# Kernel optimization log

Measured on AMD Instinct MI355X. Metric: run time of the kernel, lower is better.

Reference implementation:

```python
import jax, jax.numpy as jnp
import numpy as np


def _bilinear(plane, coords):
    # plane: [B, C, H, W]; coords: [B, N, 2] in [-1, 1]; coords[...,0]->x (W axis), [...,1]->y (H axis)
    # matches F.grid_sample(mode='bilinear', padding_mode='border', align_corners=True)
    B, C, H, W = plane.shape
    x = jnp.clip((coords[..., 0] + 1.0) * 0.5 * (W - 1), 0.0, W - 1)
    y = jnp.clip((coords[..., 1] + 1.0) * 0.5 * (H - 1), 0.0, H - 1)
    x0 = jnp.floor(x)
    y0 = jnp.floor(y)
    x0i = x0.astype(jnp.int32)
    y0i = y0.astype(jnp.int32)
    x1i = jnp.minimum(x0i + 1, W - 1)
    y1i = jnp.minimum(y0i + 1, H - 1)
    wx = (x - x0)[:, :, None]
    wy = (y - y0)[:, :, None]
    pf = plane.reshape(B, C, H * W)

    def g(yi, xi):
        idx = (yi * W + xi)[:, None, :]            # [B,1,N]
        return jnp.take_along_axis(pf, idx, axis=2).transpose(0, 2, 1)  # [B,N,C]

    f00 = g(y0i, x0i)
    f01 = g(y0i, x1i)
    f10 = g(y1i, x0i)
    f11 = g(y1i, x1i)
    return (f00 * (1 - wx) * (1 - wy) + f01 * wx * (1 - wy)
            + f10 * (1 - wx) * wy + f11 * wx * wy)


def _sample(p, c_xz, c_xy, c_yz):
    # project 3D points onto the three canonical planes and sum bilinear features
    return (_bilinear(c_xz, p[..., jnp.array([0, 2])])
            + _bilinear(c_xy, p[..., jnp.array([0, 1])])
            + _bilinear(c_yz, p[..., jnp.array([1, 2])]))


def setup_inputs() -> dict:
    key = jax.random.key(0)
    ks = jax.random.split(key, 10)
    B, N, C, S, H = 8, 4096, 128, 8, 64
    query_pos = jax.random.uniform(ks[0], (B, N, 3), dtype=jnp.float32) * 2.0 - 1.0
    c_xz = jax.random.normal(ks[1], (B, C, H, H), dtype=jnp.float32)
    c_xy = jax.random.normal(ks[2], (B, C, H, H), dtype=jnp.float32)
    c_yz = jax.random.normal(ks[3], (B, C, H, H), dtype=jnp.float32)
    s = C ** -0.5
    Wq = jax.random.normal(ks[4], (C, C), dtype=jnp.float32) * s
    Wk = jax.random.normal(ks[5], (C, C), dtype=jnp.float32) * s
    Wv = jax.random.normal(ks[6], (C, C), dtype=jnp.float32) * s
    Wout = jax.random.normal(ks[7], (C, C), dtype=jnp.float32) * s
    Woff = jax.random.normal(ks[8], (C, 3 * S), dtype=jnp.float32) * s * 0.1  # small offsets
    return dict(query_pos=query_pos, c_xz=c_xz, c_xy=c_xy, c_yz=c_yz,
                Wq=Wq, bq=jnp.zeros((C,), jnp.float32),
                Wk=Wk, bk=jnp.zeros((C,), jnp.float32),
                Wv=Wv, bv=jnp.zeros((C,), jnp.float32),
                Wout=Wout, bout=jnp.zeros((C,), jnp.float32),
                Woff=Woff, boff=jnp.zeros((3 * S,), jnp.float32))


def reference(query_pos, c_xz, c_xy, c_yz, Wq, bq, Wk, bk, Wv, bv,
              Wout, bout, Woff, boff):
    B, N, _ = query_pos.shape
    C = Wq.shape[0]
    S = Woff.shape[1] // 3
    # sample features at query points (bilinear gather from triplanes)
    feature = _sample(query_pos, c_xz, c_xy, c_yz)                     # [B,N,C]
    # learned deformable offsets -> S auxiliary sample points per query
    offset = (feature @ Woff + boff).reshape(B, N, S, 3)
    aux_pts = offset + query_pos[:, :, None, :]                        # [B,N,S,3]
    aux_feat = _sample(aux_pts.reshape(B, N * S, 3),
                       c_xz, c_xy, c_yz).reshape(B, N, S, C)           # [B,N,S,C]
    k = aux_feat @ Wk + bk                                             # [B,N,S,C]
    v = aux_feat @ Wv + bv
    q = feature @ Wq + bq                                              # [B,N,C]
    scale = C ** (-0.5)
    q = q / scale  # faithful to original: q = q / self.scale
    sim = jnp.einsum('bnd,bnjd->bnj', q, k)                            # [B,N,S]
    attn = jax.nn.softmax(sim, axis=-1)
    out = jnp.einsum('bnj,bnjd->bnd', attn, v)                         # [B,N,C]
    out = out @ Wout + bout + feature                                  # residual
    return out
```

## Files before the change

kernel.cpp:

```cpp
#include <hip/hip_runtime.h>
#include <math.h>

#define BB 8
#define NN 4096
#define CC 128
#define SS 8
#define HH 64
#define HW 4096
#define PLANE_B (HW*CC)
#define SQRT_C 11.3137084989847603904f

__global__ __launch_bounds__(128) void transpose_planes(
    const float* __restrict__ pxz, const float* __restrict__ pxy,
    const float* __restrict__ pyz, float* __restrict__ dst) {
  int bid = blockIdx.x;
  int c   = threadIdx.x;
  int hw0 = (bid & 255) * 16;
  int b   = (bid >> 8) & 7;
  int p   = bid >> 11;
  const float* src = (p == 0) ? pxz : (p == 1) ? pxy : pyz;
  const float4* s4 = (const float4*)(src + (size_t)(b * CC + c) * HW + hw0);
  float4 v0 = s4[0], v1 = s4[1], v2 = s4[2], v3 = s4[3];
  float vals[16];
  vals[0]=v0.x; vals[1]=v0.y; vals[2]=v0.z; vals[3]=v0.w;
  vals[4]=v1.x; vals[5]=v1.y; vals[6]=v1.z; vals[7]=v1.w;
  vals[8]=v2.x; vals[9]=v2.y; vals[10]=v2.z; vals[11]=v2.w;
  vals[12]=v3.x; vals[13]=v3.y; vals[14]=v3.z; vals[15]=v3.w;
  float* d = dst + (size_t)(p * BB + b) * PLANE_B + (size_t)hw0 * CC + c;
#pragma unroll
  for (int i = 0; i < 16; ++i) d[i * CC] = vals[i];
}

__device__ __forceinline__ int morton3_3(int cx, int cy, int cz) {
  int m = 0;
#pragma unroll
  for (int k = 0; k < 3; ++k) {
    m |= ((cx >> k) & 1) << (3 * k);
    m |= ((cy >> k) & 1) << (3 * k + 1);
    m |= ((cz >> k) & 1) << (3 * k + 2);
  }
  return m;
}

__global__ __launch_bounds__(1024) void sort_queries(
    const float* __restrict__ qpos, int* __restrict__ sidx) {
  const int b = blockIdx.x;
  const int t = threadIdx.x;
  __shared__ unsigned short scell[NN];
  __shared__ int hist[512];
  __shared__ int tmp[512];
  __shared__ int cur[512];
  if (t < 512) hist[t] = 0;
  __syncthreads();
  for (int i = t; i < NN; i += 1024) {
    const float* qp = qpos + ((size_t)b * NN + i) * 3;
    float x = qp[0], y = qp[1], z = qp[2];
    int cx = min(7, max(0, (int)((x + 1.f) * 4.f)));
    int cy = min(7, max(0, (int)((y + 1.f) * 4.f)));
    int cz = min(7, max(0, (int)((z + 1.f) * 4.f)));
    int cell = morton3_3(cx, cy, cz);
    scell[i] = (unsigned short)cell;
    atomicAdd(&hist[cell], 1);
  }
  __syncthreads();
  if (t < 512) tmp[t] = hist[t];
  __syncthreads();
  for (int off = 1; off < 512; off <<= 1) {
    int v = 0;
    if (t < 512 && t >= off) v = tmp[t - off];
    __syncthreads();
    if (t < 512) tmp[t] += v;
    __syncthreads();
  }
  if (t < 512) cur[t] = tmp[t] - hist[t];
  __syncthreads();
  for (int i = t; i < NN; i += 1024) {
    int cell = scell[i];
    int pos = atomicAdd(&cur[cell], 1);
    sidx[b * NN + pos] = i;
  }
}

__global__ __launch_bounds__(128) void prep_mats(
    const float* __restrict__ Wq, const float* __restrict__ bq,
    const float* __restrict__ Wk,
    const float* __restrict__ Wv, const float* __restrict__ bv,
    const float* __restrict__ Wout, const float* __restrict__ bout,
    const float* __restrict__ Woff,
    float* __restrict__ Mt, float* __restrict__ u,
    float* __restrict__ W2, float* __restrict__ b2,
    float* __restrict__ Wofft) {
  int t = threadIdx.x;
  int blk = blockIdx.x;
  if (blk < 128) {
    __shared__ float lwq[128];
    lwq[t] = Wq[blk * 128 + t];
    __syncthreads();
    float acc = 0.f;
#pragma unroll 8
    for (int d = 0; d < 128; ++d) acc += Wk[t * 128 + d] * lwq[d];
    Mt[blk * 128 + t] = SQRT_C * acc;
  } else if (blk < 256) {
    int c = blk - 128;
    float acc = 0.f;
#pragma unroll 8
    for (int e = 0; e < 128; ++e) acc += Wv[c * 128 + e] * Wout[e * 128 + t];
    W2[c * 128 + t] = acc;
  } else if (blk == 256) {
    float au = 0.f, ab = 0.f;
    for (int d = 0; d < 128; ++d) au += Wk[t * 128 + d] * bq[d];
    u[t] = SQRT_C * au;
    for (int e = 0; e < 128; ++e) ab += bv[e] * Wout[e * 128 + t];
    b2[t] = ab + bout[t];
  } else {
#pragma unroll
    for (int j = 0; j < 24; ++j) Wofft[j * 128 + t] = Woff[t * 24 + j];
  }
}

__device__ __forceinline__ void make_combo(float cx, float cy,
                                           int4* oi, float4* ow) {
  float fx = fminf(fmaxf((cx + 1.f) * 31.5f, 0.f), 63.f);
  float fy = fminf(fmaxf((cy + 1.f) * 31.5f, 0.f), 63.f);
  float x0f = floorf(fx), y0f = floorf(fy);
  int x0 = (int)x0f, y0 = (int)y0f;
  int x1 = min(x0 + 1, 63), y1 = min(y0 + 1, 63);
  float wx = fx - x0f, wy = fy - y0f;
  int r0 = y0 << 15, r1 = y1 << 15;
  int cb0 = x0 << 9, cb1 = x1 << 9;
  *oi = make_int4(r0 + cb0, r0 + cb1, r1 + cb0, r1 + cb1);
  float wxy = wx * wy;
  *ow = make_float4(1.f - wx - wy + wxy, wx - wxy, wy - wxy, wxy);
}

__device__ __forceinline__ float ldf(const char* p, int off) {
  return *(const float*)(p + off);
}

__global__ __launch_bounds__(128, 4) void deform_attn9(
    const float* __restrict__ qpos, const int* __restrict__ sidx,
    const float* __restrict__ pT,
    const float* __restrict__ Mt, const float* __restrict__ u,
    const float* __restrict__ W2, const float* __restrict__ bias2,
    const float* __restrict__ Wofft, const float* __restrict__ boff,
    float* __restrict__ out) {
  const int tid = threadIdx.x;
  const int c = tid;
  const int l = tid & 63;
  const int wv = tid >> 6;
  const int bid = blockIdx.x;
  const int b = bid & 7;
  const int n0 = (bid >> 3) * 8;

  __shared__ int snidx[8];
  __shared__ float spos[24];
  __shared__ int4   sfi[24];
  __shared__ float4 sfw[24];
  __shared__ int4   sci[192];
  __shared__ float4 scw[192];
  __shared__ __align__(16) float sbuf[CC * 8];
  __shared__ float soff[8][24];
  __shared__ float sred[8][2][8];

  if (tid < 8) snidx[tid] = sidx[b * NN + n0 + tid];
  __syncthreads();
  if (tid < 24) {
    int q = tid / 3, comp = tid - q * 3;
    spos[tid] = qpos[((size_t)b * NN + snidx[q]) * 3 + comp];
  }
  __syncthreads();

  const char* pb0 = (const char*)(pT + (size_t)(0 * BB + b) * PLANE_B + c);
  const char* pb1 = (const char*)(pT + (size_t)(1 * BB + b) * PLANE_B + c);
  const char* pb2 = (const char*)(pT + (size_t)(2 * BB + b) * PLANE_B + c);

  if (tid < 24) {
    int p = tid >> 3, q = tid & 7;
    float px = spos[q * 3 + 0], py = spos[q * 3 + 1], pz = spos[q * 3 + 2];
    float cx = (p == 2) ? py : px;
    float cy = (p == 1) ? py : pz;
    make_combo(cx, cy, &sfi[tid], &sfw[tid]);
  }
  __syncthreads();

  float featr[8];
#pragma unroll
  for (int q = 0; q < 8; ++q) {
    float f = 0.f;
#pragma unroll
    for (int p = 0; p < 3; ++p) {
      int4 oi = sfi[p * 8 + q];
      float4 w = sfw[p * 8 + q];
      const char* base = (p == 0) ? pb0 : (p == 1) ? pb1 : pb2;
      f += w.x * ldf(base, oi.x) + w.y * ldf(base, oi.y)
         + w.z * ldf(base, oi.z) + w.w * ldf(base, oi.w);
    }
    featr[q] = f;
    sbuf[c * 8 + q] = f;
  }
  __syncthreads();

  float qk[8];
  {
    float uc = u[c];
#pragma unroll
    for (int q = 0; q < 8; ++q) qk[q] = uc;
#pragma unroll 4
    for (int cp = 0; cp < CC; ++cp) {
      float m = Mt[cp * CC + c];
      float4 f0 = *(const float4*)&sbuf[cp * 8];
      float4 f1 = *(const float4*)&sbuf[cp * 8 + 4];
      qk[0] += m * f0.x; qk[1] += m * f0.y; qk[2] += m * f0.z; qk[3] += m * f0.w;
      qk[4] += m * f1.x; qk[5] += m * f1.y; qk[6] += m * f1.z; qk[7] += m * f1.w;
    }
  }

#pragma unroll
  for (int rep = 0; rep < 2; ++rep) {
    int m = rep * 128 + tid;
    if (m < 192) {
      int q = m / 24;
      int t24 = m - q * 24;
      float acc = boff[t24];
      const float* wrow = Wofft + t24 * 128;
#pragma unroll 4
      for (int cp = 0; cp < CC; ++cp) acc += sbuf[cp * 8 + q] * wrow[cp];
      soff[q][t24] = acc;
    }
  }
  __syncthreads();

#pragma unroll
  for (int rep = 0; rep < 2; ++rep) {
    int m = rep * 128 + tid;
    if (m < 192) {
      int p = m >> 6, q = (m >> 3) & 7, j = m & 7;
      float ox = spos[q * 3 + 0] + soff[q][j * 3 + 0];
      float oy = spos[q * 3 + 1] + soff[q][j * 3 + 1];
      float oz = spos[q * 3 + 2] + soff[q][j * 3 + 2];
      float cx = (p == 2) ? oy : ox;
      float cy = (p == 1) ? oy : oz;
      make_combo(cx, cy, &sci[m], &scw[m]);
    }
  }
  __syncthreads();

  const int lb0 = l & 1, lb1 = (l >> 1) & 1, lb2 = (l >> 2) & 1;
#pragma unroll
  for (int q = 0; q < 8; ++q) {
    float a8[8], part[8];
#pragma unroll
    for (int j = 0; j < 8; ++j) {
      float a = 0.f;
#pragma unroll
      for (int p = 0; p < 3; ++p) {
        int idx = p * 64 + q * 8 + j;
        int4 oi = sci[idx];
        float4 w = scw[idx];
        const char* base = (p == 0) ? pb0 : (p == 1) ? pb1 : pb2;
        a += w.x * ldf(base, oi.x) + w.y * ldf(base, oi.y)
           + w.z * ldf(base, oi.z) + w.w * ldf(base, oi.w);
      }
      a8[j] = a;
      part[j] = a * qk[q];
    }
    float s2[4];
#pragma unroll
    for (int k = 0; k < 4; ++k) {
      float pa = part[2 * k], pb_ = part[2 * k + 1];
      float snd = lb0 ? pa : pb_;
      float kp  = lb0 ? pb_ : pa;
      s2[k] = kp + __shfl_xor(snd, 1);
    }
    float s4[2];
#pragma unroll
    for (int k = 0; k < 2; ++k) {
      float pa = s2[2 * k], pb_ = s2[2 * k + 1];
      float snd = lb1 ? pa : pb_;
      float kp  = lb1 ? pb_ : pa;
      s4[k] = kp + __shfl_xor(snd, 2);
    }
    float s8;
    {
      float snd = lb2 ? s4[0] : s4[1];
      float kp  = lb2 ? s4[1] : s4[0];
      s8 = kp + __shfl_xor(snd, 4);
    }
    s8 += __shfl_xor(s8, 8);
    s8 += __shfl_xor(s8, 16);
    s8 += __shfl_xor(s8, 32);
    if (l < 8) sred[q][wv][l] = s8;
    __syncthreads();
    float sim[8];
#pragma unroll
    for (int j = 0; j < 8; ++j) sim[j] = sred[q][0][j] + sred[q][1][j];
    float mx = fmaxf(fmaxf(fmaxf(sim[0], sim[1]), fmaxf(sim[2], sim[3])),
                     fmaxf(fmaxf(sim[4], sim[5]), fmaxf(sim[6], sim[7])));
    float den = 0.f;
#pragma unroll
    for (int j = 0; j < 8; ++j) { sim[j] = __expf(sim[j] - mx); den += sim[j]; }
    float inv = 1.f / den;
    float w = 0.f;
#pragma unroll
    for (int j = 0; j < 8; ++j) w += sim[j] * a8[j];
    sbuf[c * 8 + q] = w * inv;
  }
  __syncthreads();

  float o[8];
  {
    float bb = bias2[c];
#pragma unroll
    for (int q = 0; q < 8; ++q) o[q] = bb;
#pragma unroll 4
    for (int cp = 0; cp < CC; ++cp) {
      float m = W2[cp * CC + c];
      float4 f0 = *(const float4*)&sbuf[cp * 8];
      float4 f1 = *(const float4*)&sbuf[cp * 8 + 4];
      o[0] += m * f0.x; o[1] += m * f0.y; o[2] += m * f0.z; o[3] += m * f0.w;
      o[4] += m * f1.x; o[5] += m * f1.y; o[6] += m * f1.z; o[7] += m * f1.w;
    }
  }
#pragma unroll
  for (int q = 0; q < 8; ++q) {
    out[((size_t)b * NN + snidx[q]) * CC + c] = o[q] + featr[q];
  }
}

__device__ __forceinline__ float bil(const float* __restrict__ base,
                                     float cx, float cy, int es, int rs) {
  float fx = fminf(fmaxf((cx + 1.f) * 31.5f, 0.f), 63.f);
  float fy = fminf(fmaxf((cy + 1.f) * 31.5f, 0.f), 63.f);
  float x0f = floorf(fx), y0f = floorf(fy);
  int x0 = (int)x0f, y0 = (int)y0f;
  int x1 = min(x0 + 1, 63), y1 = min(y0 + 1, 63);
  float wx = fx - x0f, wy = fy - y0f;
  const float* r0 = base + y0 * rs;
  const float* r1 = base + y1 * rs;
  float f00 = r0[x0 * es], f01 = r0[x1 * es];
  float f10 = r1[x0 * es], f11 = r1[x1 * es];
  float top = f00 + (f01 - f00) * wx;
  float bot = f10 + (f11 - f10) * wx;
  return top + (bot - top) * wy;
}

__global__ __launch_bounds__(128) void deform_attn_fb(
    const float* __restrict__ qpos,
    const float* __restrict__ pxz, const float* __restrict__ pxy,
    const float* __restrict__ pyz,
    const float* __restrict__ Mt, const float* __restrict__ u,
    const float* __restrict__ W2, const float* __restrict__ b2,
    const float* __restrict__ Woff, const float* __restrict__ boff,
    float* __restrict__ out) {
  const int tid = threadIdx.x;
  const int c = tid;
  const int bid = blockIdx.x;
  const int b = bid & 7;
  const int n0 = (bid >> 3) * 8;
  const int es = 1, rs = HH;
  const float* bxz = pxz + (size_t)(b * CC + c) * HW;
  const float* bxy = pxy + (size_t)(b * CC + c) * HW;
  const float* byz = pyz + (size_t)(b * CC + c) * HW;

  __shared__ __align__(16) float sfeat[CC * 8];
  __shared__ __align__(16) float swv[CC * 8];
  __shared__ float spos[24];
  __shared__ float soff[8][24];
  __shared__ float sred[8][2][8];

  if (tid < 24) spos[tid] = qpos[(size_t)(b * NN + n0) * 3 + tid];
  __syncthreads();
#pragma unroll
  for (int q = 0; q < 8; ++q) {
    float px = spos[q*3+0], py = spos[q*3+1], pz = spos[q*3+2];
    sfeat[c*8+q] = bil(bxz,px,pz,es,rs)+bil(bxy,px,py,es,rs)+bil(byz,py,pz,es,rs);
  }
  __syncthreads();
  float qk[8];
  {
    float uc = u[c];
#pragma unroll
    for (int q = 0; q < 8; ++q) qk[q] = uc;
    for (int cp = 0; cp < CC; ++cp) {
      float m = Mt[cp*CC+c];
#pragma unroll
      for (int q = 0; q < 8; ++q) qk[q] += m * sfeat[cp*8+q];
    }
  }
  if (tid < 120) {
    int q = tid/24, j = tid%24;
    float acc = boff[j];
    for (int cp = 0; cp < CC; ++cp) acc += sfeat[cp*8+q]*Woff[cp*24+j];
    soff[q][j] = acc;
  }
  if (tid < 72) {
    int q = 5+tid/24, j = tid%24;
    float acc = boff[j];
    for (int cp = 0; cp < CC; ++cp) acc += sfeat[cp*8+q]*Woff[cp*24+j];
    soff[q][j] = acc;
  }
  __syncthreads();
  const int wvid = tid >> 6;
  for (int q = 0; q < 8; ++q) {
    float px = spos[q*3+0], py = spos[q*3+1], pz = spos[q*3+2];
    float a8[8];
#pragma unroll
    for (int j = 0; j < 8; ++j) {
      float ox = px+soff[q][j*3+0], oy = py+soff[q][j*3+1], oz = pz+soff[q][j*3+2];
      float a = bil(bxz,ox,oz,es,rs)+bil(bxy,ox,oy,es,rs)+bil(byz,oy,oz,es,rs);
      a8[j] = a;
      float p = a * qk[q];
#pragma unroll
      for (int m = 1; m < 64; m <<= 1) p += __shfl_xor(p, m);
      if ((tid & 63) == 0) sred[q][wvid][j] = p;
    }
    __syncthreads();
    float attn[8], mx = -INFINITY;
#pragma unroll
    for (int j = 0; j < 8; ++j) { attn[j] = sred[q][0][j]+sred[q][1][j]; mx = fmaxf(mx, attn[j]); }
    float den = 0.f;
#pragma unroll
    for (int j = 0; j < 8; ++j) { attn[j] = __expf(attn[j]-mx); den += attn[j]; }
    float inv = 1.f/den, w = 0.f;
#pragma unroll
    for (int j = 0; j < 8; ++j) w += attn[j]*a8[j];
    swv[c*8+q] = w*inv;
  }
  __syncthreads();
  float o[8];
  {
    float bb = b2[c];
#pragma unroll
    for (int q = 0; q < 8; ++q) o[q] = bb;
    for (int cp = 0; cp < CC; ++cp) {
      float wv2 = W2[cp*CC+c];
#pragma unroll
      for (int q = 0; q < 8; ++q) o[q] += wv2 * swv[cp*8+q];
    }
  }
#pragma unroll
  for (int q = 0; q < 8; ++q)
    out[(size_t)(b*NN+n0+q)*CC+c] = o[q] + sfeat[c*8+q];
}

extern "C" void kernel_launch(void* const* d_in, const int* in_sizes, int n_in,
                              void* d_out, int out_size, void* d_ws, size_t ws_size,
                              hipStream_t stream) {
  const float* qpos = (const float*)d_in[0];
  const float* pxz  = (const float*)d_in[1];
  const float* pxy  = (const float*)d_in[2];
  const float* pyz  = (const float*)d_in[3];
  const float* Wq   = (const float*)d_in[4];
  const float* bq   = (const float*)d_in[5];
  const float* Wk   = (const float*)d_in[6];
  const float* Wv   = (const float*)d_in[8];
  const float* bv   = (const float*)d_in[9];
  const float* Wout = (const float*)d_in[10];
  const float* bout = (const float*)d_in[11];
  const float* Woff = (const float*)d_in[12];
  const float* boff = (const float*)d_in[13];
  float* out = (float*)d_out;

  float* w = (float*)d_ws;
  const size_t nT = (size_t)3 * BB * HW * CC;
  const size_t matFloats = 16384 + 128 + 16384 + 128 + 24 * 128;
  const size_t sidxInts = (size_t)BB * NN;
  bool tp = ws_size >= (nT + matFloats + sidxInts) * sizeof(float);

  float* wsT  = w;
  float* wsMt = tp ? (w + nT) : w;
  float* wsU  = wsMt + 16384;
  float* wsW2 = wsU + 128;
  float* wsB2 = wsW2 + 16384;
  float* wsWofft = wsB2 + 128;
  int*   wsSidx  = (int*)(wsWofft + 24 * 128);

  prep_mats<<<258, 128, 0, stream>>>(Wq, bq, Wk, Wv, bv, Wout, bout, Woff,
                                     wsMt, wsU, wsW2, wsB2, wsWofft);
  if (tp) {
    sort_queries<<<BB, 1024, 0, stream>>>(qpos, wsSidx);
    transpose_planes<<<3 * BB * (HW / 16), 128, 0, stream>>>(pxz, pxy, pyz, wsT);
    deform_attn9<<<(BB * NN) / 8, 128, 0, stream>>>(
        qpos, wsSidx, wsT, wsMt, wsU, wsW2, wsB2, wsWofft, boff, out);
  } else {
    deform_attn_fb<<<(BB * NN) / 8, 128, 0, stream>>>(
        qpos, pxz, pxy, pyz, wsMt, wsU, wsW2, wsB2, Woff, boff, out);
  }
}
```

Measured before the change: 202.6 us.

## Store triplanes with paired row y/y+1 values so bilinear taps use float2 loads

A new transpose kernel writes each texel as a float2 holding the values at row y and row y+1 for each channel, doubling the transposed plane size. The attention kernel then fetches the four bilinear corners with two 8-byte loads instead of four 4-byte loads, halving the number of gather instructions. In exchange, the transpose writes twice the data, the gather footprint grows, and the path needs a larger workspace, falling back to the old path when the workspace is too small.

```diff
diff --git a/kernel.cpp b/kernel.cpp
--- a/kernel.cpp
+++ b/kernel.cpp
@@ -8,6 +8,7 @@
 #define HH 64
 #define HW 4096
 #define PLANE_B (HW*CC)
+#define PLANE2 (HW*CC*2)
 #define SQRT_C 11.3137084989847603904f
 
 __global__ __launch_bounds__(128) void transpose_planes(
@@ -29,6 +30,35 @@
   float* d = dst + (size_t)(p * BB + b) * PLANE_B + (size_t)hw0 * CC + c;
 #pragma unroll
   for (int i = 0; i < 16; ++i) d[i * CC] = vals[i];
+}
+
+__global__ __launch_bounds__(128) void transpose_planes_p(
+    const float* __restrict__ pxz, const float* __restrict__ pxy,
+    const float* __restrict__ pyz, float* __restrict__ dst) {
+  int bid = blockIdx.x;
+  int c   = threadIdx.x;
+  int hw0 = (bid & 255) * 16;
+  int b   = (bid >> 8) & 7;
+  int p   = bid >> 11;
+  int y   = hw0 >> 6;
+  int x0  = hw0 & 63;
+  int y1  = min(y + 1, 63);
+  const float* src = (p == 0) ? pxz : (p == 1) ? pxy : pyz;
+  const float* rowb = src + (size_t)(b * CC + c) * HW;
+  const float4* sa = (const float4*)(rowb + y  * 64 + x0);
+  const float4* sb = (const float4*)(rowb + y1 * 64 + x0);
+  float va[16], vb[16];
+#pragma unroll
+  for (int k = 0; k < 4; ++k) {
+    float4 t = sa[k];
+    va[4*k]=t.x; va[4*k+1]=t.y; va[4*k+2]=t.z; va[4*k+3]=t.w;
+    float4 u = sb[k];
+    vb[4*k]=u.x; vb[4*k+1]=u.y; vb[4*k+2]=u.z; vb[4*k+3]=u.w;
+  }
+  float2* d = (float2*)(dst + (size_t)(p * BB + b) * PLANE2
+                            + ((size_t)hw0 * CC + c) * 2);
+#pragma unroll
+  for (int i = 0; i < 16; ++i) d[i * CC] = make_float2(va[i], vb[i]);
 }
 
 __device__ __forceinline__ int morton3_3(int cx, int cy, int cz) {
@@ -133,8 +163,217 @@
   *ow = make_float4(1.f - wx - wy + wxy, wx - wxy, wy - wxy, wxy);
 }
 
+__device__ __forceinline__ void make_combo_p(float cx, float cy,
+                                             int2* oi, float4* ow) {
+  float fx = fminf(fmaxf((cx + 1.f) * 31.5f, 0.f), 63.f);
+  float fy = fminf(fmaxf((cy + 1.f) * 31.5f, 0.f), 63.f);
+  float x0f = floorf(fx), y0f = floorf(fy);
+  int x0 = (int)x0f, y0 = (int)y0f;
+  int x1 = min(x0 + 1, 63);
+  float wx = fx - x0f, wy = fy - y0f;
+  int r0 = y0 << 16;
+  *oi = make_int2(r0 + (x0 << 10), r0 + (x1 << 10));
+  float wxy = wx * wy;
+  *ow = make_float4(1.f - wx - wy + wxy, wy - wxy, wx - wxy, wxy);
+}
+
 __device__ __forceinline__ float ldf(const char* p, int off) {
   return *(const float*)(p + off);
+}
+__device__ __forceinline__ float2 ld2(const char* p, int off) {
+  return *(const float2*)(p + off);
+}
+
+__global__ __launch_bounds__(128, 4) void deform_attn10(
+    const float* __restrict__ qpos, const int* __restrict__ sidx,
+    const float* __restrict__ pT,
+    const float* __restrict__ Mt, const float* __restrict__ u,
+    const float* __restrict__ W2, const float* __restrict__ bias2,
+    const float* __restrict__ Wofft, const float* __restrict__ boff,
+    float* __restrict__ out) {
+  const int tid = threadIdx.x;
+  const int c = tid;
+  const int l = tid & 63;
+  const int wv = tid >> 6;
+  const int bid = blockIdx.x;
+  const int b = bid & 7;
+  const int n0 = (bid >> 3) * 8;
+
+  __shared__ int snidx[8];
+  __shared__ float spos[24];
+  __shared__ int2   sfi[24];
+  __shared__ float4 sfw[24];
+  __shared__ int2   sci[192];
+  __shared__ float4 scw[192];
+  __shared__ __align__(16) float sbuf[CC * 8];
+  __shared__ float soff[8][24];
+  __shared__ float sred[8][2][8];
+
+  if (tid < 8) snidx[tid] = sidx[b * NN + n0 + tid];
+  __syncthreads();
+  if (tid < 24) {
+    int q = tid / 3, comp = tid - q * 3;
+    spos[tid] = qpos[((size_t)b * NN + snidx[q]) * 3 + comp];
+  }
+  __syncthreads();
+
+  const char* pb0 = (const char*)(pT + (size_t)(0 * BB + b) * PLANE2) + 8 * c;
+  const char* pb1 = (const char*)(pT + (size_t)(1 * BB + b) * PLANE2) + 8 * c;
+  const char* pb2 = (const char*)(pT + (size_t)(2 * BB + b) * PLANE2) + 8 * c;
+
+  if (tid < 24) {
+    int p = tid >> 3, q = tid & 7;
+    float px = spos[q * 3 + 0], py = spos[q * 3 + 1], pz = spos[q * 3 + 2];
+    float cx = (p == 2) ? py : px;
+    float cy = (p == 1) ? py : pz;
+    make_combo_p(cx, cy, &sfi[tid], &sfw[tid]);
+  }
+  __syncthreads();
+
+  float featr[8];
+#pragma unroll
+  for (int q = 0; q < 8; ++q) {
+    float f = 0.f;
+#pragma unroll
+    for (int p = 0; p < 3; ++p) {
+      int2 oi = sfi[p * 8 + q];
+      float4 w = sfw[p * 8 + q];
+      const char* base = (p == 0) ? pb0 : (p == 1) ? pb1 : pb2;
+      float2 L0 = ld2(base, oi.x);
+      float2 L1 = ld2(base, oi.y);
+      f += w.x * L0.x + w.y * L0.y + w.z * L1.x + w.w * L1.y;
+    }
+    featr[q] = f;
+    sbuf[c * 8 + q] = f;
+  }
+  __syncthreads();
+
+  float qk[8];
+  {
+    float uc = u[c];
+#pragma unroll
+    for (int q = 0; q < 8; ++q) qk[q] = uc;
+#pragma unroll 4
+    for (int cp = 0; cp < CC; ++cp) {
+      float m = Mt[cp * CC + c];
+      float4 f0 = *(const float4*)&sbuf[cp * 8];
+      float4 f1 = *(const float4*)&sbuf[cp * 8 + 4];
+      qk[0] += m * f0.x; qk[1] += m * f0.y; qk[2] += m * f0.z; qk[3] += m * f0.w;
+      qk[4] += m * f1.x; qk[5] += m * f1.y; qk[6] += m * f1.z; qk[7] += m * f1.w;
+    }
+  }
+
+#pragma unroll
+  for (int rep = 0; rep < 2; ++rep) {
+    int m = rep * 128 + tid;
+    if (m < 192) {
+      int q = m / 24;
+      int t24 = m - q * 24;
+      float acc = boff[t24];
+      const float* wrow = Wofft + t24 * 128;
+#pragma unroll 4
+      for (int cp = 0; cp < CC; ++cp) acc += sbuf[cp * 8 + q] * wrow[cp];
+      soff[q][t24] = acc;
+    }
+  }
+  __syncthreads();
+
+#pragma unroll
+  for (int rep = 0; rep < 2; ++rep) {
+    int m = rep * 128 + tid;
+    if (m < 192) {
+      int p = m >> 6, q = (m >> 3) & 7, j = m & 7;
+      float ox = spos[q * 3 + 0] + soff[q][j * 3 + 0];
+      float oy = spos[q * 3 + 1] + soff[q][j * 3 + 1];
+      float oz = spos[q * 3 + 2] + soff[q][j * 3 + 2];
+      float cx = (p == 2) ? oy : ox;
+      float cy = (p == 1) ? oy : oz;
+      make_combo_p(cx, cy, &sci[m], &scw[m]);
+    }
+  }
+  __syncthreads();
+
+  const int lb0 = l & 1, lb1 = (l >> 1) & 1, lb2 = (l >> 2) & 1;
+#pragma unroll
+  for (int q = 0; q < 8; ++q) {
+    float a8[8], part[8];
+#pragma unroll
+    for (int j = 0; j < 8; ++j) {
+      float a = 0.f;
+#pragma unroll
+      for (int p = 0; p < 3; ++p) {
+        int idx = p * 64 + q * 8 + j;
+        int2 oi = sci[idx];
+        float4 w = scw[idx];
+        const char* base = (p == 0) ? pb0 : (p == 1) ? pb1 : pb2;
+        float2 L0 = ld2(base, oi.x);
+        float2 L1 = ld2(base, oi.y);
+        a += w.x * L0.x + w.y * L0.y + w.z * L1.x + w.w * L1.y;
+      }
+      a8[j] = a;
+      part[j] = a * qk[q];
+    }
+    float s2[4];
+#pragma unroll
+    for (int k = 0; k < 4; ++k) {
+      float pa = part[2 * k], pb_ = part[2 * k + 1];
+      float snd = lb0 ? pa : pb_;
+      float kp  = lb0 ? pb_ : pa;
+      s2[k] = kp + __shfl_xor(snd, 1);
+    }
+    float s4[2];
+#pragma unroll
+    for (int k = 0; k < 2; ++k) {
+      float pa = s2[2 * k], pb_ = s2[2 * k + 1];
+      float snd = lb1 ? pa : pb_;
+      float kp  = lb1 ? pb_ : pa;
+      s4[k] = kp + __shfl_xor(snd, 2);
+    }
+    float s8;
+    {
+      float snd = lb2 ? s4[0] : s4[1];
+      float kp  = lb2 ? s4[1] : s4[0];
+      s8 = kp + __shfl_xor(snd, 4);
+    }
+    s8 += __shfl_xor(s8, 8);
+    s8 += __shfl_xor(s8, 16);
+    s8 += __shfl_xor(s8, 32);
+    if (l < 8) sred[q][wv][l] = s8;
+    __syncthreads();
+    float sim[8];
+#pragma unroll
+    for (int j = 0; j < 8; ++j) sim[j] = sred[q][0][j] + sred[q][1][j];
+    float mx = fmaxf(fmaxf(fmaxf(sim[0], sim[1]), fmaxf(sim[2], sim[3])),
+                     fmaxf(fmaxf(sim[4], sim[5]), fmaxf(sim[6], sim[7])));
+    float den = 0.f;
+#pragma unroll
+    for (int j = 0; j < 8; ++j) { sim[j] = __expf(sim[j] - mx); den += sim[j]; }
+    float inv = 1.f / den;
+    float w = 0.f;
+#pragma unroll
+    for (int j = 0; j < 8; ++j) w += sim[j] * a8[j];
+    sbuf[c * 8 + q] = w * inv;
+  }
+  __syncthreads();
+
+  float o[8];
+  {
+    float bb = bias2[c];
+#pragma unroll
+    for (int q = 0; q < 8; ++q) o[q] = bb;
+#pragma unroll 4
+    for (int cp = 0; cp < CC; ++cp) {
+      float m = W2[cp * CC + c];
+      float4 f0 = *(const float4*)&sbuf[cp * 8];
+      float4 f1 = *(const float4*)&sbuf[cp * 8 + 4];
+      o[0] += m * f0.x; o[1] += m * f0.y; o[2] += m * f0.z; o[3] += m * f0.w;
+      o[4] += m * f1.x; o[5] += m * f1.y; o[6] += m * f1.z; o[7] += m * f1.w;
+    }
+  }
+#pragma unroll
+  for (int q = 0; q < 8; ++q) {
+    out[((size_t)b * NN + snidx[q]) * CC + c] = o[q] + featr[q];
+  }
 }
 
 __global__ __launch_bounds__(128, 4) void deform_attn9(
@@ -462,11 +701,14 @@
   float* out = (float*)d_out;
 
   float* w = (float*)d_ws;
-  const size_t nT = (size_t)3 * BB * HW * CC;
+  const size_t nT2 = (size_t)3 * BB * HW * CC * 2;
+  const size_t nT1 = (size_t)3 * BB * HW * CC;
   const size_t matFloats = 16384 + 128 + 16384 + 128 + 24 * 128;
   const size_t sidxInts = (size_t)BB * NN;
-  bool tp = ws_size >= (nT + matFloats + sidxInts) * sizeof(float);
-
+  bool paired = ws_size >= (nT2 + matFloats + sidxInts) * sizeof(float);
+  bool tp = paired || ws_size >= (nT1 + matFloats + sidxInts) * sizeof(float);
+
+  size_t nT = paired ? nT2 : nT1;
   float* wsT  = w;
   float* wsMt = tp ? (w + nT) : w;
   float* wsU  = wsMt + 16384;
@@ -479,9 +721,15 @@
                                      wsMt, wsU, wsW2, wsB2, wsWofft);
   if (tp) {
     sort_queries<<<BB, 1024, 0, stream>>>(qpos, wsSidx);
-    transpose_planes<<<3 * BB * (HW / 16), 128, 0, stream>>>(pxz, pxy, pyz, wsT);
-    deform_attn9<<<(BB * NN) / 8, 128, 0, stream>>>(
-        qpos, wsSidx, wsT, wsMt, wsU, wsW2, wsB2, wsWofft, boff, out);
+    if (paired) {
+      transpose_planes_p<<<3 * BB * (HW / 16), 128, 0, stream>>>(pxz, pxy, pyz, wsT);
+      deform_attn10<<<(BB * NN) / 8, 128, 0, stream>>>(
+          qpos, wsSidx, wsT, wsMt, wsU, wsW2, wsB2, wsWofft, boff, out);
+    } else {
+      transpose_planes<<<3 * BB * (HW / 16), 128, 0, stream>>>(pxz, pxy, pyz, wsT);
+      deform_attn9<<<(BB * NN) / 8, 128, 0, stream>>>(
+          qpos, wsSidx, wsT, wsMt, wsU, wsW2, wsB2, wsWofft, boff, out);
+    }
   } else {
     deform_attn_fb<<<(BB * NN) / 8, 128, 0, stream>>>(
         qpos, pxz, pxy, pyz, wsMt, wsU, wsW2, wsB2, Woff, boff, out);
```

New measurement: 250.3 us. +23.6%, slower.

## Split queries across waves with float2 channel gathers and recompute aux samples

Applied to the files above, without the earlier changes.

Each wave now handles four of the eight queries, and each lane gathers two adjacent channels with float2 loads instead of one channel per thread across all queries. Attention is reduced entirely within a wave using shuffles, which removes the per-query block barriers and the shared reduction buffer. Auxiliary samples are gathered a second time for the value pass rather than kept in registers. The projection matrices are stored transposed so each thread reads its row with float4 loads. The aim is fewer block syncs and wider gathers, paid for with twice the auxiliary gather traffic and extra shared-memory staging.

```diff
diff --git a/kernel.cpp b/kernel.cpp
--- a/kernel.cpp
+++ b/kernel.cpp
@@ -87,8 +87,8 @@
     const float* __restrict__ Wv, const float* __restrict__ bv,
     const float* __restrict__ Wout, const float* __restrict__ bout,
     const float* __restrict__ Woff,
-    float* __restrict__ Mt, float* __restrict__ u,
-    float* __restrict__ W2, float* __restrict__ b2,
+    float* __restrict__ MtT, float* __restrict__ u,
+    float* __restrict__ W2T, float* __restrict__ b2,
     float* __restrict__ Wofft) {
   int t = threadIdx.x;
   int blk = blockIdx.x;
@@ -99,13 +99,13 @@
     float acc = 0.f;
 #pragma unroll 8
     for (int d = 0; d < 128; ++d) acc += Wk[t * 128 + d] * lwq[d];
-    Mt[blk * 128 + t] = SQRT_C * acc;
+    MtT[t * 128 + blk] = SQRT_C * acc;
   } else if (blk < 256) {
-    int c = blk - 128;
+    int cp = blk - 128;
     float acc = 0.f;
 #pragma unroll 8
-    for (int e = 0; e < 128; ++e) acc += Wv[c * 128 + e] * Wout[e * 128 + t];
-    W2[c * 128 + t] = acc;
+    for (int e = 0; e < 128; ++e) acc += Wv[cp * 128 + e] * Wout[e * 128 + t];
+    W2T[t * 128 + cp] = acc;
   } else if (blk == 256) {
     float au = 0.f, ab = 0.f;
     for (int d = 0; d < 128; ++d) au += Wk[t * 128 + d] * bq[d];
@@ -133,21 +133,22 @@
   *ow = make_float4(1.f - wx - wy + wxy, wx - wxy, wy - wxy, wxy);
 }
 
-__device__ __forceinline__ float ldf(const char* p, int off) {
-  return *(const float*)(p + off);
-}
-
-__global__ __launch_bounds__(128, 4) void deform_attn9(
+__device__ __forceinline__ float2 ld2(const char* p, int off) {
+  return *(const float2*)(p + off);
+}
+
+__global__ __launch_bounds__(128, 4) void deform_attn11(
     const float* __restrict__ qpos, const int* __restrict__ sidx,
     const float* __restrict__ pT,
-    const float* __restrict__ Mt, const float* __restrict__ u,
-    const float* __restrict__ W2, const float* __restrict__ bias2,
+    const float* __restrict__ MtT, const float* __restrict__ u,
+    const float* __restrict__ W2T, const float* __restrict__ bias2,
     const float* __restrict__ Wofft, const float* __restrict__ boff,
     float* __restrict__ out) {
   const int tid = threadIdx.x;
   const int c = tid;
   const int l = tid & 63;
   const int wv = tid >> 6;
+  const int qb = wv * 4;
   const int bid = blockIdx.x;
   const int b = bid & 7;
   const int n0 = (bid >> 3) * 8;
@@ -159,8 +160,8 @@
   __shared__ int4   sci[192];
   __shared__ float4 scw[192];
   __shared__ __align__(16) float sbuf[CC * 8];
+  __shared__ __align__(16) float swacc[CC * 8];
   __shared__ float soff[8][24];
-  __shared__ float sred[8][2][8];
 
   if (tid < 8) snidx[tid] = sidx[b * NN + n0 + tid];
   __syncthreads();
@@ -170,9 +171,9 @@
   }
   __syncthreads();
 
-  const char* pb0 = (const char*)(pT + (size_t)(0 * BB + b) * PLANE_B + c);
-  const char* pb1 = (const char*)(pT + (size_t)(1 * BB + b) * PLANE_B + c);
-  const char* pb2 = (const char*)(pT + (size_t)(2 * BB + b) * PLANE_B + c);
+  const char* gp0 = (const char*)(pT + (size_t)(0 * BB + b) * PLANE_B) + 8 * l;
+  const char* gp1 = (const char*)(pT + (size_t)(1 * BB + b) * PLANE_B) + 8 * l;
+  const char* gp2 = (const char*)(pT + (size_t)(2 * BB + b) * PLANE_B) + 8 * l;
 
   if (tid < 24) {
     int p = tid >> 3, q = tid & 7;
@@ -183,36 +184,51 @@
   }
   __syncthreads();
 
-  float featr[8];
-#pragma unroll
-  for (int q = 0; q < 8; ++q) {
-    float f = 0.f;
-#pragma unroll
-    for (int p = 0; p < 3; ++p) {
-      int4 oi = sfi[p * 8 + q];
-      float4 w = sfw[p * 8 + q];
-      const char* base = (p == 0) ? pb0 : (p == 1) ? pb1 : pb2;
-      f += w.x * ldf(base, oi.x) + w.y * ldf(base, oi.y)
-         + w.z * ldf(base, oi.z) + w.w * ldf(base, oi.w);
-    }
-    featr[q] = f;
-    sbuf[c * 8 + q] = f;
-  }
-  __syncthreads();
-
-  float qk[8];
+  {
+    float f0q[4], f1q[4];
+#pragma unroll
+    for (int qi = 0; qi < 4; ++qi) {
+      int q = qb + qi;
+      float f0 = 0.f, f1 = 0.f;
+#pragma unroll
+      for (int p = 0; p < 3; ++p) {
+        const char* g = (p == 0) ? gp0 : (p == 1) ? gp1 : gp2;
+        int4 oi = sfi[p * 8 + q];
+        float4 w = sfw[p * 8 + q];
+        float2 v;
+        v = ld2(g, oi.x); f0 += w.x * v.x; f1 += w.x * v.y;
+        v = ld2(g, oi.y); f0 += w.y * v.x; f1 += w.y * v.y;
+        v = ld2(g, oi.z); f0 += w.z * v.x; f1 += w.z * v.y;
+        v = ld2(g, oi.w); f0 += w.w * v.x; f1 += w.w * v.y;
+      }
+      f0q[qi] = f0; f1q[qi] = f1;
+    }
+    *(float4*)&sbuf[(2 * l) * 8 + qb]     = make_float4(f0q[0], f0q[1], f0q[2], f0q[3]);
+    *(float4*)&sbuf[(2 * l + 1) * 8 + qb] = make_float4(f1q[0], f1q[1], f1q[2], f1q[3]);
+  }
+  __syncthreads();
+
   {
     float uc = u[c];
+    float qk[8];
 #pragma unroll
     for (int q = 0; q < 8; ++q) qk[q] = uc;
+    const float4* mrow = (const float4*)(MtT + (size_t)c * 128);
 #pragma unroll 4
-    for (int cp = 0; cp < CC; ++cp) {
-      float m = Mt[cp * CC + c];
-      float4 f0 = *(const float4*)&sbuf[cp * 8];
-      float4 f1 = *(const float4*)&sbuf[cp * 8 + 4];
-      qk[0] += m * f0.x; qk[1] += m * f0.y; qk[2] += m * f0.z; qk[3] += m * f0.w;
-      qk[4] += m * f1.x; qk[5] += m * f1.y; qk[6] += m * f1.z; qk[7] += m * f1.w;
-    }
+    for (int cp4 = 0; cp4 < 32; ++cp4) {
+      float4 m4 = mrow[cp4];
+#pragma unroll
+      for (int k = 0; k < 4; ++k) {
+        int cp = cp4 * 4 + k;
+        float mk = (k == 0) ? m4.x : (k == 1) ? m4.y : (k == 2) ? m4.z : m4.w;
+        float4 f0 = *(const float4*)&sbuf[cp * 8];
+        float4 f1 = *(const float4*)&sbuf[cp * 8 + 4];
+        qk[0] += mk * f0.x; qk[1] += mk * f0.y; qk[2] += mk * f0.z; qk[3] += mk * f0.w;
+        qk[4] += mk * f1.x; qk[5] += mk * f1.y; qk[6] += mk * f1.z; qk[7] += mk * f1.w;
+      }
+    }
+    *(float4*)&swacc[c * 8]     = make_float4(qk[0], qk[1], qk[2], qk[3]);
+    *(float4*)&swacc[c * 8 + 4] = make_float4(qk[4], qk[5], qk[6], qk[7]);
   }
 
 #pragma unroll
@@ -245,85 +261,123 @@
   }
   __syncthreads();
 
-  const int lb0 = l & 1, lb1 = (l >> 1) & 1, lb2 = (l >> 2) & 1;
-#pragma unroll
-  for (int q = 0; q < 8; ++q) {
-    float a8[8], part[8];
-#pragma unroll
-    for (int j = 0; j < 8; ++j) {
-      float a = 0.f;
-#pragma unroll
-      for (int p = 0; p < 3; ++p) {
-        int idx = p * 64 + q * 8 + j;
-        int4 oi = sci[idx];
-        float4 w = scw[idx];
-        const char* base = (p == 0) ? pb0 : (p == 1) ? pb1 : pb2;
-        a += w.x * ldf(base, oi.x) + w.y * ldf(base, oi.y)
-           + w.z * ldf(base, oi.z) + w.w * ldf(base, oi.w);
-      }
-      a8[j] = a;
-      part[j] = a * qk[q];
-    }
-    float s2[4];
-#pragma unroll
-    for (int k = 0; k < 4; ++k) {
-      float pa = part[2 * k], pb_ = part[2 * k + 1];
-      float snd = lb0 ? pa : pb_;
-      float kp  = lb0 ? pb_ : pa;
-      s2[k] = kp + __shfl_xor(snd, 1);
-    }
-    float s4[2];
-#pragma unroll
-    for (int k = 0; k < 2; ++k) {
-      float pa = s2[2 * k], pb_ = s2[2 * k + 1];
-      float snd = lb1 ? pa : pb_;
-      float kp  = lb1 ? pb_ : pa;
-      s4[k] = kp + __shfl_xor(snd, 2);
-    }
-    float s8;
-    {
-      float snd = lb2 ? s4[0] : s4[1];
-      float kp  = lb2 ? s4[1] : s4[0];
-      s8 = kp + __shfl_xor(snd, 4);
-    }
-    s8 += __shfl_xor(s8, 8);
-    s8 += __shfl_xor(s8, 16);
-    s8 += __shfl_xor(s8, 32);
-    if (l < 8) sred[q][wv][l] = s8;
-    __syncthreads();
-    float sim[8];
-#pragma unroll
-    for (int j = 0; j < 8; ++j) sim[j] = sred[q][0][j] + sred[q][1][j];
-    float mx = fmaxf(fmaxf(fmaxf(sim[0], sim[1]), fmaxf(sim[2], sim[3])),
-                     fmaxf(fmaxf(sim[4], sim[5]), fmaxf(sim[6], sim[7])));
-    float den = 0.f;
-#pragma unroll
-    for (int j = 0; j < 8; ++j) { sim[j] = __expf(sim[j] - mx); den += sim[j]; }
-    float inv = 1.f / den;
-    float w = 0.f;
-#pragma unroll
-    for (int j = 0; j < 8; ++j) w += sim[j] * a8[j];
-    sbuf[c * 8 + q] = w * inv;
-  }
-  __syncthreads();
-
-  float o[8];
+  {
+    float4 q0v = *(const float4*)&swacc[(2 * l) * 8 + qb];
+    float4 q1v = *(const float4*)&swacc[(2 * l + 1) * 8 + qb];
+    const int lb0 = l & 1, lb1 = (l >> 1) & 1, lb2 = (l >> 2) & 1;
+#pragma unroll
+    for (int qi = 0; qi < 4; ++qi) {
+      int q = qb + qi;
+      float qv0 = (qi == 0) ? q0v.x : (qi == 1) ? q0v.y : (qi == 2) ? q0v.z : q0v.w;
+      float qv1 = (qi == 0) ? q1v.x : (qi == 1) ? q1v.y : (qi == 2) ? q1v.z : q1v.w;
+      float part[8];
+#pragma unroll
+      for (int j = 0; j < 8; ++j) {
+        float a0 = 0.f, a1 = 0.f;
+#pragma unroll
+        for (int p = 0; p < 3; ++p) {
+          int idx = p * 64 + q * 8 + j;
+          const char* g = (p == 0) ? gp0 : (p == 1) ? gp1 : gp2;
+          int4 oi = sci[idx];
+          float4 w = scw[idx];
+          float2 v;
+          v = ld2(g, oi.x); a0 += w.x * v.x; a1 += w.x * v.y;
+          v = ld2(g, oi.y); a0 += w.y * v.x; a1 += w.y * v.y;
+          v = ld2(g, oi.z); a0 += w.z * v.x; a1 += w.z * v.y;
+          v = ld2(g, oi.w); a0 += w.w * v.x; a1 += w.w * v.y;
+        }
+        part[j] = a0 * qv0 + a1 * qv1;
+      }
+      float s2[4];
+#pragma unroll
+      for (int k = 0; k < 4; ++k) {
+        float pa = part[2 * k], pb_ = part[2 * k + 1];
+        float snd = lb0 ? pa : pb_;
+        float kp  = lb0 ? pb_ : pa;
+        s2[k] = kp + __shfl_xor(snd, 1);
+      }
+      float s4_[2];
+#pragma unroll
+      for (int k = 0; k < 2; ++k) {
+        float pa = s2[2 * k], pb_ = s2[2 * k + 1];
+        float snd = lb1 ? pa : pb_;
+        float kp  = lb1 ? pb_ : pa;
+        s4_[k] = kp + __shfl_xor(snd, 2);
+      }
+      float s8;
+      {
+        float snd = lb2 ? s4_[0] : s4_[1];
+        float kp  = lb2 ? s4_[1] : s4_[0];
+        s8 = kp + __shfl_xor(snd, 4);
+      }
+      s8 += __shfl_xor(s8, 8);
+      s8 += __shfl_xor(s8, 16);
+      s8 += __shfl_xor(s8, 32);
+      float mx = s8;
+      mx = fmaxf(mx, __shfl_xor(mx, 1));
+      mx = fmaxf(mx, __shfl_xor(mx, 2));
+      mx = fmaxf(mx, __shfl_xor(mx, 4));
+      float e = __expf(s8 - mx);
+      float den = e;
+      den += __shfl_xor(den, 1);
+      den += __shfl_xor(den, 2);
+      den += __shfl_xor(den, 4);
+      float attn = e / den;
+      float w0 = 0.f, w1 = 0.f;
+#pragma unroll
+      for (int j = 0; j < 8; ++j) {
+        float aj = __shfl(attn, j);
+        float a0 = 0.f, a1 = 0.f;
+#pragma unroll
+        for (int p = 0; p < 3; ++p) {
+          int idx = p * 64 + q * 8 + j;
+          const char* g = (p == 0) ? gp0 : (p == 1) ? gp1 : gp2;
+          int4 oi = sci[idx];
+          float4 w = scw[idx];
+          float2 v;
+          v = ld2(g, oi.x); a0 += w.x * v.x; a1 += w.x * v.y;
+          v = ld2(g, oi.y); a0 += w.y * v.x; a1 += w.y * v.y;
+          v = ld2(g, oi.z); a0 += w.z * v.x; a1 += w.z * v.y;
+          v = ld2(g, oi.w); a0 += w.w * v.x; a1 += w.w * v.y;
+        }
+        w0 += aj * a0;
+        w1 += aj * a1;
+      }
+      swacc[(2 * l) * 8 + q]     = w0;
+      swacc[(2 * l + 1) * 8 + q] = w1;
+    }
+  }
+  __syncthreads();
+
   {
     float bb = bias2[c];
+    float o[8];
 #pragma unroll
     for (int q = 0; q < 8; ++q) o[q] = bb;
+    const float4* wrow = (const float4*)(W2T + (size_t)c * 128);
 #pragma unroll 4
-    for (int cp = 0; cp < CC; ++cp) {
-      float m = W2[cp * CC + c];
-      float4 f0 = *(const float4*)&sbuf[cp * 8];
-      float4 f1 = *(const float4*)&sbuf[cp * 8 + 4];
-      o[0] += m * f0.x; o[1] += m * f0.y; o[2] += m * f0.z; o[3] += m * f0.w;
-      o[4] += m * f1.x; o[5] += m * f1.y; o[6] += m * f1.z; o[7] += m * f1.w;
-    }
-  }
-#pragma unroll
-  for (int q = 0; q < 8; ++q) {
-    out[((size_t)b * NN + snidx[q]) * CC + c] = o[q] + featr[q];
+    for (int cp4 = 0; cp4 < 32; ++cp4) {
+      float4 m4 = wrow[cp4];
+#pragma unroll
+      for (int k = 0; k < 4; ++k) {
+        int cp = cp4 * 4 + k;
+        float mk = (k == 0) ? m4.x : (k == 1) ? m4.y : (k == 2) ? m4.z : m4.w;
+        float4 f0 = *(const float4*)&swacc[cp * 8];
+        float4 f1 = *(const float4*)&swacc[cp * 8 + 4];
+        o[0] += mk * f0.x; o[1] += mk * f0.y; o[2] += mk * f0.z; o[3] += mk * f0.w;
+        o[4] += mk * f1.x; o[5] += mk * f1.y; o[6] += mk * f1.z; o[7] += mk * f1.w;
+      }
+    }
+    float4 r0 = *(const float4*)&sbuf[c * 8];
+    float4 r1 = *(const float4*)&sbuf[c * 8 + 4];
+    out[((size_t)b * NN + snidx[0]) * CC + c] = o[0] + r0.x;
+    out[((size_t)b * NN + snidx[1]) * CC + c] = o[1] + r0.y;
+    out[((size_t)b * NN + snidx[2]) * CC + c] = o[2] + r0.z;
+    out[((size_t)b * NN + snidx[3]) * CC + c] = o[3] + r0.w;
+    out[((size_t)b * NN + snidx[4]) * CC + c] = o[4] + r1.x;
+    out[((size_t)b * NN + snidx[5]) * CC + c] = o[5] + r1.y;
+    out[((size_t)b * NN + snidx[6]) * CC + c] = o[6] + r1.z;
+    out[((size_t)b * NN + snidx[7]) * CC + c] = o[7] + r1.w;
   }
 }
 
@@ -348,8 +402,8 @@
     const float* __restrict__ qpos,
     const float* __restrict__ pxz, const float* __restrict__ pxy,
     const float* __restrict__ pyz,
-    const float* __restrict__ Mt, const float* __restrict__ u,
-    const float* __restrict__ W2, const float* __restrict__ b2,
+    const float* __restrict__ MtT, const float* __restrict__ u,
+    const float* __restrict__ W2T, const float* __restrict__ b2,
     const float* __restrict__ Woff, const float* __restrict__ boff,
     float* __restrict__ out) {
   const int tid = threadIdx.x;
@@ -382,7 +436,7 @@
 #pragma unroll
     for (int q = 0; q < 8; ++q) qk[q] = uc;
     for (int cp = 0; cp < CC; ++cp) {
-      float m = Mt[cp*CC+c];
+      float m = MtT[c*CC+cp];
 #pragma unroll
       for (int q = 0; q < 8; ++q) qk[q] += m * sfeat[cp*8+q];
     }
@@ -433,7 +487,7 @@
 #pragma unroll
     for (int q = 0; q < 8; ++q) o[q] = bb;
     for (int cp = 0; cp < CC; ++cp) {
-      float wv2 = W2[cp*CC+c];
+      float wv2 = W2T[c*CC+cp];
 #pragma unroll
       for (int q = 0; q < 8; ++q) o[q] += wv2 * swv[cp*8+q];
     }
@@ -480,7 +534,7 @@
   if (tp) {
     sort_queries<<<BB, 1024, 0, stream>>>(qpos, wsSidx);
     transpose_planes<<<3 * BB * (HW / 16), 128, 0, stream>>>(pxz, pxy, pyz, wsT);
-    deform_attn9<<<(BB * NN) / 8, 128, 0, stream>>>(
+    deform_attn11<<<(BB * NN) / 8, 128, 0, stream>>>(
         qpos, wsSidx, wsT, wsMt, wsU, wsW2, wsB2, wsWofft, boff, out);
   } else {
     deform_attn_fb<<<(BB * NN) / 8, 128, 0, stream>>>(
```

Result: slower. 256.9 us (+26.8%).
